# Performance work log

Hardware: AMD Instinct MI355X
Metric: run time of the kernel (lower is better)

Reference implementation:

```python
import jax, jax.numpy as jnp
import numpy as np

T = 4096          # tokens (batch*seq)
D = 768           # moe_intermediate_size (token hidden dim)
I = 2048          # intermediate_size (FFN inner dim)
E = 8             # num_experts


def setup_inputs() -> dict:
    key = jax.random.key(0)
    k_x, k_p, k_g, k_u, k_d = jax.random.split(key, 5)
    hidden_states = jax.random.normal(k_x, (T, D), dtype=jnp.float32)
    position_index = jax.random.randint(k_p, (T,), 0, E, dtype=jnp.int64)
    behavior_index = jnp.zeros((T,), dtype=jnp.int64)  # unused (behavior_injection=False)
    s = 0.02
    # torch Linear weight layout: [out_features, in_features]
    gate_w = jax.random.normal(k_g, (E, I, D), dtype=jnp.float32) * s
    up_w = jax.random.normal(k_u, (E, I, D), dtype=jnp.float32) * s
    down_w = jax.random.normal(k_d, (E, D, I), dtype=jnp.float32) * s
    return {
        "hidden_states": hidden_states,
        "position_index": position_index,
        "behavior_index": behavior_index,
        "gate_w": gate_w,
        "up_w": up_w,
        "down_w": down_w,
    }


def reference(hidden_states, position_index, behavior_index, gate_w, up_w, down_w):
    # Sparse MoE dispatch: each token routed to exactly one expert by position_index.
    # Dropout rate is 0.0 (eval) -> identity. behavior_injection=False -> behavior_index unused.
    num_experts = gate_w.shape[0]
    out = jnp.zeros_like(hidden_states)
    for e in range(num_experts):  # structural loop over fixed expert count
        mask = (position_index == e)[:, None]          # [T, 1]
        g = hidden_states @ gate_w[e].T                 # [T, I]
        u = hidden_states @ up_w[e].T                   # [T, I]
        y = (jax.nn.silu(g) * u) @ down_w[e].T          # [T, D]
        out = out + jnp.where(mask, y, 0.0)             # scatter-combine
    return out
```

## Files before the change

### kernel.cpp

```cpp
#include <hip/hip_runtime.h>
#include <hip/hip_bf16.h>

#define T_TOK 4096
#define DDIM  768
#define IDIM  2048
#define NEXP  8
#define LSTR  40
#define LSTR2 72

typedef __attribute__((ext_vector_type(8))) short  bfrag;
typedef __attribute__((ext_vector_type(4))) float  ffrag;

static __device__ __forceinline__ unsigned short f2bf(float f) {
    union { float f; unsigned u; } v; v.f = f;
    unsigned r = v.u + 0x7FFFu + ((v.u >> 16) & 1u);
    return (unsigned short)(r >> 16);
}

static __device__ __forceinline__ unsigned cvt2(float x, float y) {
    union { __hip_bfloat162 h; unsigned u; } v;
    v.h = __float22bfloat162_rn(make_float2(x, y));
    return v.u;
}

static __device__ __forceinline__ uint4 cvt8(float4 a, float4 b) {
    uint4 o;
    o.x = cvt2(a.x, a.y); o.y = cvt2(a.z, a.w);
    o.z = cvt2(b.x, b.y); o.w = cvt2(b.z, b.w);
    return o;
}

#define PIPE_BAR() do { \
    asm volatile("s_waitcnt lgkmcnt(0)" ::: "memory"); \
    __builtin_amdgcn_s_barrier(); \
    __builtin_amdgcn_sched_barrier(0); \
} while (0)

__global__ void k_sort(const int* __restrict__ pos, int* __restrict__ ws_i,
                       int* __restrict__ perm) {
    __shared__ int hist[NEXP], cursor[NEXP];
    const int tid = threadIdx.x;
    if (tid < NEXP) hist[tid] = 0;
    __syncthreads();
    for (int i = tid; i < T_TOK; i += 1024)
        atomicAdd(&hist[pos[i]], 1);
    __syncthreads();
    if (tid == 0) {
        int s = 0;
        for (int e = 0; e < NEXP; ++e) {
            cursor[e] = s;
            ws_i[e] = hist[e];
            ws_i[16 + e] = s;
            s += hist[e];
        }
        ws_i[16 + NEXP] = s;
    }
    __syncthreads();
    for (int i = tid; i < T_TOK; i += 1024) {
        int p = atomicAdd(&cursor[pos[i]], 1);
        perm[p] = i;
    }
}

__launch_bounds__(256, 3)
__global__ void k_gemm1(const float* __restrict__ x,
                        const int* __restrict__ perm,
                        const float* __restrict__ gate_w,
                        const float* __restrict__ up_w,
                        unsigned short* __restrict__ hg,
                        const int* __restrict__ ws_i) {
    const int e   = blockIdx.z;
    const int cnt = ws_i[e];
    const int m0  = blockIdx.y * 128;
    if (m0 >= cnt) return;
    const int off = ws_i[16 + e];
    const int n0  = blockIdx.x * 64;

    const int tid  = threadIdx.x;
    const int lane = tid & 63;
    const int wave = tid >> 6;
    const int wm   = wave & 1;
    const int wn   = wave >> 1;

    __shared__ __align__(16) unsigned short lsA[2][128 * LSTR];
    __shared__ __align__(16) unsigned short lsG[2][64 * LSTR];
    __shared__ __align__(16) unsigned short lsU[2][64 * LSTR];

    const float* gate_e = gate_w + (size_t)e * (IDIM * DDIM);
    const float* up_e   = up_w   + (size_t)e * (IDIM * DDIM);

    const int arow = tid >> 1, aq = tid & 1;
    const int brow = tid >> 2, bq = tid & 3;

    int trow = off + m0 + arow; if (trow > T_TOK - 1) trow = T_TOK - 1;
    const int tok = perm[trow];
    const float* ap = x + (size_t)tok * DDIM + aq * 16;
    const float* gp = gate_e + (size_t)(n0 + brow) * DDIM + bq * 8;
    const float* up = up_e   + (size_t)(n0 + brow) * DDIM + bq * 8;

    ffrag accG[4][2], accU[4][2];
    const ffrag fz = {0.f, 0.f, 0.f, 0.f};
    for (int mi = 0; mi < 4; ++mi)
        for (int ni = 0; ni < 2; ++ni) { accG[mi][ni] = fz; accU[mi][ni] = fz; }

    const int koff = (lane >> 4) * 8;
    const int rsel = lane & 15;

    float4 Pa0, Pa1, Pa2, Pa3, Pg0, Pg1, Pu0, Pu1;

#define G1_LOAD(kb) do { \
    Pa0 = *reinterpret_cast<const float4*>(ap + (kb)); \
    Pa1 = *reinterpret_cast<const float4*>(ap + (kb) + 4); \
    Pa2 = *reinterpret_cast<const float4*>(ap + (kb) + 8); \
    Pa3 = *reinterpret_cast<const float4*>(ap + (kb) + 12); \
    Pg0 = *reinterpret_cast<const float4*>(gp + (kb)); \
    Pg1 = *reinterpret_cast<const float4*>(gp + (kb) + 4); \
    Pu0 = *reinterpret_cast<const float4*>(up + (kb)); \
    Pu1 = *reinterpret_cast<const float4*>(up + (kb) + 4); } while (0)

#define G1_STORE(B) do { \
    *reinterpret_cast<uint4*>(&lsA[B][arow * LSTR + aq * 16])     = cvt8(Pa0, Pa1); \
    *reinterpret_cast<uint4*>(&lsA[B][arow * LSTR + aq * 16 + 8]) = cvt8(Pa2, Pa3); \
    *reinterpret_cast<uint4*>(&lsG[B][brow * LSTR + bq * 8]) = cvt8(Pg0, Pg1); \
    *reinterpret_cast<uint4*>(&lsU[B][brow * LSTR + bq * 8]) = cvt8(Pu0, Pu1); } while (0)

#define G1_COMPUTE(B) do { \
    bfrag a[4], bg[2], bu[2]; \
    _Pragma("unroll") \
    for (int mi = 0; mi < 4; ++mi) \
        a[mi] = *reinterpret_cast<const bfrag*>(&lsA[B][(wm * 64 + mi * 16 + rsel) * LSTR + koff]); \
    _Pragma("unroll") \
    for (int ni = 0; ni < 2; ++ni) { \
        bg[ni] = *reinterpret_cast<const bfrag*>(&lsG[B][(wn * 32 + ni * 16 + rsel) * LSTR + koff]); \
        bu[ni] = *reinterpret_cast<const bfrag*>(&lsU[B][(wn * 32 + ni * 16 + rsel) * LSTR + koff]); \
    } \
    _Pragma("unroll") \
    for (int mi = 0; mi < 4; ++mi) { \
        _Pragma("unroll") \
        for (int ni = 0; ni < 2; ++ni) { \
            accG[mi][ni] = __builtin_amdgcn_mfma_f32_16x16x32_bf16(a[mi], bg[ni], accG[mi][ni], 0, 0, 0); \
            accU[mi][ni] = __builtin_amdgcn_mfma_f32_16x16x32_bf16(a[mi], bu[ni], accU[mi][ni], 0, 0, 0); \
        } \
    } } while (0)

    G1_LOAD(0);
    G1_STORE(0);
    G1_LOAD(32);
    PIPE_BAR();

    #pragma unroll 2
    for (int kt = 0; kt < 24; ++kt) {
        const int cur = kt & 1;
        if (kt < 23) G1_STORE(cur ^ 1);
        if (kt < 22) G1_LOAD((kt + 2) * 32);
        G1_COMPUTE(cur);
        PIPE_BAR();
    }
#undef G1_LOAD
#undef G1_STORE
#undef G1_COMPUTE

    const int colb  = lane & 15;
    const int rquad = (lane >> 4) * 4;
    #pragma unroll
    for (int mi = 0; mi < 4; ++mi)
        #pragma unroll
        for (int ni = 0; ni < 2; ++ni) {
            int n = n0 + wn * 32 + ni * 16 + colb;
            #pragma unroll
            for (int r = 0; r < 4; ++r) {
                int ml = wm * 64 + mi * 16 + rquad + r;
                if (m0 + ml < cnt) {
                    float g = accG[mi][ni][r];
                    float u = accU[mi][ni][r];
                    float h = (g / (1.0f + __expf(-g))) * u;
                    hg[(size_t)(off + m0 + ml) * IDIM + n] = f2bf(h);
                }
            }
        }
}

__launch_bounds__(256, 4)
__global__ void k_gemm2(const unsigned short* __restrict__ hg,
                        const float* __restrict__ down_w,
                        float* __restrict__ out,
                        const int* __restrict__ ws_i,
                        const int* __restrict__ perm) {
    const int e   = blockIdx.z;
    const int cnt = ws_i[e];
    const int m0  = blockIdx.y * 64;
    if (m0 >= cnt) return;
    const int off = ws_i[16 + e];
    const int n0  = blockIdx.x * 64;

    const int tid  = threadIdx.x;
    const int lane = tid & 63;
    const int wave = tid >> 6;
    const int wm   = wave & 1;
    const int wn   = wave >> 1;

    __shared__ __align__(16) unsigned short lsA[2][64 * LSTR2];
    __shared__ __align__(16) unsigned short lsB[2][64 * LSTR2];

    const float* down_e = down_w + (size_t)e * (DDIM * IDIM);

    const int arow = tid >> 2, aq = tid & 3;

    int g0 = off + m0 + arow; if (g0 > T_TOK - 1) g0 = T_TOK - 1;
    const unsigned short* ap = hg + (size_t)g0 * IDIM + aq * 16;
    const float* bp = down_e + (size_t)(n0 + arow) * IDIM + aq * 16;

    ffrag acc[2][2];
    const ffrag fz = {0.f, 0.f, 0.f, 0.f};
    for (int mi = 0; mi < 2; ++mi)
        for (int ni = 0; ni < 2; ++ni) acc[mi][ni] = fz;

    const int koff = (lane >> 4) * 8;
    const int rsel = lane & 15;

    uint4  Pa0, Pa1;
    float4 Pb0, Pb1, Pb2, Pb3;

#define G2_LOAD(kb) do { \
    Pa0 = *reinterpret_cast<const uint4*>(ap + (kb)); \
    Pa1 = *reinterpret_cast<const uint4*>(ap + (kb) + 8); \
    Pb0 = *reinterpret_cast<const float4*>(bp + (kb)); \
    Pb1 = *reinterpret_cast<const float4*>(bp + (kb) + 4); \
    Pb2 = *reinterpret_cast<const float4*>(bp + (kb) + 8); \
    Pb3 = *reinterpret_cast<const float4*>(bp + (kb) + 12); } while (0)

#define G2_STORE(B) do { \
    *reinterpret_cast<uint4*>(&lsA[B][arow * LSTR2 + aq * 16])     = Pa0; \
    *reinterpret_cast<uint4*>(&lsA[B][arow * LSTR2 + aq * 16 + 8]) = Pa1; \
    *reinterpret_cast<uint4*>(&lsB[B][arow * LSTR2 + aq * 16])     = cvt8(Pb0, Pb1); \
    *reinterpret_cast<uint4*>(&lsB[B][arow * LSTR2 + aq * 16 + 8]) = cvt8(Pb2, Pb3); } while (0)

#define G2_COMPUTE(B) do { \
    _Pragma("unroll") \
    for (int h = 0; h < 2; ++h) { \
        const int ko = h * 32 + koff; \
        bfrag a[2], b[2]; \
        _Pragma("unroll") \
        for (int mi = 0; mi < 2; ++mi) \
            a[mi] = *reinterpret_cast<const bfrag*>(&lsA[B][(wm * 32 + mi * 16 + rsel) * LSTR2 + ko]); \
        _Pragma("unroll") \
        for (int ni = 0; ni < 2; ++ni) \
            b[ni] = *reinterpret_cast<const bfrag*>(&lsB[B][(wn * 32 + ni * 16 + rsel) * LSTR2 + ko]); \
        _Pragma("unroll") \
        for (int mi = 0; mi < 2; ++mi) { \
            _Pragma("unroll") \
            for (int ni = 0; ni < 2; ++ni) \
                acc[mi][ni] = __builtin_amdgcn_mfma_f32_16x16x32_bf16(a[mi], b[ni], acc[mi][ni], 0, 0, 0); \
        } \
    } } while (0)

    G2_LOAD(0);
    G2_STORE(0);
    G2_LOAD(64);
    PIPE_BAR();

    #pragma unroll 2
    for (int kt = 0; kt < 32; ++kt) {
        const int cur = kt & 1;
        if (kt < 31) G2_STORE(cur ^ 1);
        if (kt < 30) G2_LOAD((kt + 2) * 64);
        G2_COMPUTE(cur);
        PIPE_BAR();
    }
#undef G2_LOAD
#undef G2_STORE
#undef G2_COMPUTE

    const int colb  = lane & 15;
    const int rquad = (lane >> 4) * 4;
    #pragma unroll
    for (int mi = 0; mi < 2; ++mi)
        #pragma unroll
        for (int ni = 0; ni < 2; ++ni) {
            int n = n0 + wn * 32 + ni * 16 + colb;
            #pragma unroll
            for (int r = 0; r < 4; ++r) {
                int ml = wm * 32 + mi * 16 + rquad + r;
                if (m0 + ml < cnt) {
                    int tok = perm[off + m0 + ml];
                    out[(size_t)tok * DDIM + n] = acc[mi][ni][r];
                }
            }
        }
}

extern "C" void kernel_launch(void* const* d_in, const int* in_sizes, int n_in,
                              void* d_out, int out_size, void* d_ws, size_t ws_size,
                              hipStream_t stream) {
    const float* x      = (const float*)d_in[0];
    const int*   pos    = (const int*)d_in[1];
    const float* gate_w = (const float*)d_in[3];
    const float* up_w   = (const float*)d_in[4];
    const float* down_w = (const float*)d_in[5];
    float* out = (float*)d_out;

    char* ws = (char*)d_ws;
    int* ws_i = (int*)ws;
    int* perm = (int*)(ws + 1024);
    unsigned short* hg = (unsigned short*)(ws + 32768);

    k_sort<<<dim3(1), dim3(1024), 0, stream>>>(pos, ws_i, perm);

    dim3 g1(IDIM / 64, T_TOK / 128, NEXP);
    k_gemm1<<<g1, dim3(256), 0, stream>>>(x, perm, gate_w, up_w, hg, ws_i);
    dim3 g2(DDIM / 64, T_TOK / 64, NEXP);
    k_gemm2<<<g2, dim3(256), 0, stream>>>(hg, down_w, out, ws_i, perm);
}
```

Before: 285.8 us.

## Deepen global prefetch to two stages with register double-buffering in both GEMMs

Both GEMM kernels now hold two sets of prefetch registers, so global loads run two K-tiles ahead of compute instead of one. The loop is manually unrolled by two with fixed LDS buffer indices. Occupancy hints drop by one block per CU to leave room for the extra registers. In gemm2 the grid axes are swapped so M tiles map to blockIdx.x, which changes block scheduling order and reuse of down_w tiles across blocks. The trade-off is fewer resident waves in exchange for more latency hiding.

```diff
diff --git a/kernel.cpp b/kernel.cpp
--- a/kernel.cpp
+++ b/kernel.cpp
@@ -62,7 +62,7 @@
     }
 }
 
-__launch_bounds__(256, 3)
+__launch_bounds__(256, 2)
 __global__ void k_gemm1(const float* __restrict__ x,
                         const int* __restrict__ perm,
                         const float* __restrict__ gate_w,
@@ -106,23 +106,24 @@
     const int koff = (lane >> 4) * 8;
     const int rsel = lane & 15;
 
-    float4 Pa0, Pa1, Pa2, Pa3, Pg0, Pg1, Pu0, Pu1;
-
-#define G1_LOAD(kb) do { \
-    Pa0 = *reinterpret_cast<const float4*>(ap + (kb)); \
-    Pa1 = *reinterpret_cast<const float4*>(ap + (kb) + 4); \
-    Pa2 = *reinterpret_cast<const float4*>(ap + (kb) + 8); \
-    Pa3 = *reinterpret_cast<const float4*>(ap + (kb) + 12); \
-    Pg0 = *reinterpret_cast<const float4*>(gp + (kb)); \
-    Pg1 = *reinterpret_cast<const float4*>(gp + (kb) + 4); \
-    Pu0 = *reinterpret_cast<const float4*>(up + (kb)); \
-    Pu1 = *reinterpret_cast<const float4*>(up + (kb) + 4); } while (0)
-
-#define G1_STORE(B) do { \
-    *reinterpret_cast<uint4*>(&lsA[B][arow * LSTR + aq * 16])     = cvt8(Pa0, Pa1); \
-    *reinterpret_cast<uint4*>(&lsA[B][arow * LSTR + aq * 16 + 8]) = cvt8(Pa2, Pa3); \
-    *reinterpret_cast<uint4*>(&lsG[B][brow * LSTR + bq * 8]) = cvt8(Pg0, Pg1); \
-    *reinterpret_cast<uint4*>(&lsU[B][brow * LSTR + bq * 8]) = cvt8(Pu0, Pu1); } while (0)
+    float4 Aa0, Aa1, Aa2, Aa3, Ag0, Ag1, Au0, Au1;
+    float4 Ba0, Ba1, Ba2, Ba3, Bg0, Bg1, Bu0, Bu1;
+
+#define G1_LOAD(S, kb) do { \
+    S##a0 = *reinterpret_cast<const float4*>(ap + (kb)); \
+    S##a1 = *reinterpret_cast<const float4*>(ap + (kb) + 4); \
+    S##a2 = *reinterpret_cast<const float4*>(ap + (kb) + 8); \
+    S##a3 = *reinterpret_cast<const float4*>(ap + (kb) + 12); \
+    S##g0 = *reinterpret_cast<const float4*>(gp + (kb)); \
+    S##g1 = *reinterpret_cast<const float4*>(gp + (kb) + 4); \
+    S##u0 = *reinterpret_cast<const float4*>(up + (kb)); \
+    S##u1 = *reinterpret_cast<const float4*>(up + (kb) + 4); } while (0)
+
+#define G1_STORE(B, S) do { \
+    *reinterpret_cast<uint4*>(&lsA[B][arow * LSTR + aq * 16])     = cvt8(S##a0, S##a1); \
+    *reinterpret_cast<uint4*>(&lsA[B][arow * LSTR + aq * 16 + 8]) = cvt8(S##a2, S##a3); \
+    *reinterpret_cast<uint4*>(&lsG[B][brow * LSTR + bq * 8]) = cvt8(S##g0, S##g1); \
+    *reinterpret_cast<uint4*>(&lsU[B][brow * LSTR + bq * 8]) = cvt8(S##u0, S##u1); } while (0)
 
 #define G1_COMPUTE(B) do { \
     bfrag a[4], bg[2], bu[2]; \
@@ -143,18 +144,21 @@
         } \
     } } while (0)
 
-    G1_LOAD(0);
-    G1_STORE(0);
-    G1_LOAD(32);
+    G1_LOAD(A, 0);
+    G1_LOAD(B, 32);
+    G1_STORE(0, A);
     PIPE_BAR();
-
-    #pragma unroll 2
-    for (int kt = 0; kt < 24; ++kt) {
-        const int cur = kt & 1;
-        if (kt < 23) G1_STORE(cur ^ 1);
-        if (kt < 22) G1_LOAD((kt + 2) * 32);
-        G1_COMPUTE(cur);
+    G1_LOAD(A, 64);
+
+    for (int kt = 0; kt < 24; kt += 2) {
+        G1_STORE(1, B);
+        G1_COMPUTE(0);
         PIPE_BAR();
+        if (kt + 3 < 24) G1_LOAD(B, (kt + 3) * 32);
+        if (kt + 2 < 24) G1_STORE(0, A);
+        G1_COMPUTE(1);
+        PIPE_BAR();
+        if (kt + 4 < 24) G1_LOAD(A, (kt + 4) * 32);
     }
 #undef G1_LOAD
 #undef G1_STORE
@@ -180,7 +184,7 @@
         }
 }
 
-__launch_bounds__(256, 4)
+__launch_bounds__(256, 3)
 __global__ void k_gemm2(const unsigned short* __restrict__ hg,
                         const float* __restrict__ down_w,
                         float* __restrict__ out,
@@ -188,10 +192,10 @@
                         const int* __restrict__ perm) {
     const int e   = blockIdx.z;
     const int cnt = ws_i[e];
-    const int m0  = blockIdx.y * 64;
+    const int m0  = blockIdx.x * 64;
     if (m0 >= cnt) return;
     const int off = ws_i[16 + e];
-    const int n0  = blockIdx.x * 64;
+    const int n0  = blockIdx.y * 64;
 
     const int tid  = threadIdx.x;
     const int lane = tid & 63;
@@ -218,22 +222,22 @@
     const int koff = (lane >> 4) * 8;
     const int rsel = lane & 15;
 
-    uint4  Pa0, Pa1;
-    float4 Pb0, Pb1, Pb2, Pb3;
-
-#define G2_LOAD(kb) do { \
-    Pa0 = *reinterpret_cast<const uint4*>(ap + (kb)); \
-    Pa1 = *reinterpret_cast<const uint4*>(ap + (kb) + 8); \
-    Pb0 = *reinterpret_cast<const float4*>(bp + (kb)); \
-    Pb1 = *reinterpret_cast<const float4*>(bp + (kb) + 4); \
-    Pb2 = *reinterpret_cast<const float4*>(bp + (kb) + 8); \
-    Pb3 = *reinterpret_cast<const float4*>(bp + (kb) + 12); } while (0)
-
-#define G2_STORE(B) do { \
-    *reinterpret_cast<uint4*>(&lsA[B][arow * LSTR2 + aq * 16])     = Pa0; \
-    *reinterpret_cast<uint4*>(&lsA[B][arow * LSTR2 + aq * 16 + 8]) = Pa1; \
-    *reinterpret_cast<uint4*>(&lsB[B][arow * LSTR2 + aq * 16])     = cvt8(Pb0, Pb1); \
-    *reinterpret_cast<uint4*>(&lsB[B][arow * LSTR2 + aq * 16 + 8]) = cvt8(Pb2, Pb3); } while (0)
+    uint4 Xa0, Xa1; float4 Xb0, Xb1, Xb2, Xb3;
+    uint4 Ya0, Ya1; float4 Yb0, Yb1, Yb2, Yb3;
+
+#define G2_LOAD(S, kb) do { \
+    S##a0 = *reinterpret_cast<const uint4*>(ap + (kb)); \
+    S##a1 = *reinterpret_cast<const uint4*>(ap + (kb) + 8); \
+    S##b0 = *reinterpret_cast<const float4*>(bp + (kb)); \
+    S##b1 = *reinterpret_cast<const float4*>(bp + (kb) + 4); \
+    S##b2 = *reinterpret_cast<const float4*>(bp + (kb) + 8); \
+    S##b3 = *reinterpret_cast<const float4*>(bp + (kb) + 12); } while (0)
+
+#define G2_STORE(B, S) do { \
+    *reinterpret_cast<uint4*>(&lsA[B][arow * LSTR2 + aq * 16])     = S##a0; \
+    *reinterpret_cast<uint4*>(&lsA[B][arow * LSTR2 + aq * 16 + 8]) = S##a1; \
+    *reinterpret_cast<uint4*>(&lsB[B][arow * LSTR2 + aq * 16])     = cvt8(S##b0, S##b1); \
+    *reinterpret_cast<uint4*>(&lsB[B][arow * LSTR2 + aq * 16 + 8]) = cvt8(S##b2, S##b3); } while (0)
 
 #define G2_COMPUTE(B) do { \
     _Pragma("unroll") \
@@ -254,18 +258,21 @@
         } \
     } } while (0)
 
-    G2_LOAD(0);
-    G2_STORE(0);
-    G2_LOAD(64);
+    G2_LOAD(X, 0);
+    G2_LOAD(Y, 64);
+    G2_STORE(0, X);
     PIPE_BAR();
-
-    #pragma unroll 2
-    for (int kt = 0; kt < 32; ++kt) {
-        const int cur = kt & 1;
-        if (kt < 31) G2_STORE(cur ^ 1);
-        if (kt < 30) G2_LOAD((kt + 2) * 64);
-        G2_COMPUTE(cur);
+    G2_LOAD(X, 128);
+
+    for (int kt = 0; kt < 32; kt += 2) {
+        G2_STORE(1, Y);
+        G2_COMPUTE(0);
         PIPE_BAR();
+        if (kt + 3 < 32) G2_LOAD(Y, (kt + 3) * 64);
+        if (kt + 2 < 32) G2_STORE(0, X);
+        G2_COMPUTE(1);
+        PIPE_BAR();
+        if (kt + 4 < 32) G2_LOAD(X, (kt + 4) * 64);
     }
 #undef G2_LOAD
 #undef G2_STORE
@@ -308,6 +315,6 @@
 
     dim3 g1(IDIM / 64, T_TOK / 128, NEXP);
     k_gemm1<<<g1, dim3(256), 0, stream>>>(x, perm, gate_w, up_w, hg, ws_i);
-    dim3 g2(DDIM / 64, T_TOK / 64, NEXP);
+    dim3 g2(T_TOK / 64, DDIM / 64, NEXP);
     k_gemm2<<<g2, dim3(256), 0, stream>>>(hg, down_w, out, ws_i, perm);
 }
```

After: 409.4 us. 1.43x slower.
